# Kernel tuning notes

Measured on AMD Instinct MI355X. Metric: run time of the kernel, lower is better.

Reference implementation:

```python
import jax, jax.numpy as jnp
import numpy as np


def insert_tdl(tdl, x):
    # Shift delay line: newest sample at row 0, drop oldest row.
    return jnp.concatenate([x, tdl[:-1]], axis=0)


def setup_inputs() -> dict:
    key = jax.random.key(0)
    ks = jax.random.split(key, 17)
    B = 16384            # batch of parallel simulations (columns)
    H = 1024             # controller hidden size
    Hp = 1024            # plant hidden size
    Dci = Dcr = Dco = 64 # controller TDL depths
    Dpi = Dpo = 64       # plant TDL depths
    f = lambda k, s: jax.random.normal(k, s, dtype=jnp.float32)
    return {
        "reference": f(ks[0], (1, B)),
        "citdl": f(ks[1], (Dci, B)),
        "crtdl": f(ks[2], (Dcr, B)),
        "cotdl": f(ks[3], (Dco, B)),
        "pitdl": f(ks[4], (Dpi - 1, B)),  # fresh controller output a2 completes the line
        "potdl": f(ks[5], (Dpo, B)),
        # controller parameters (trainable in the original)
        "ciw": 0.01 * f(ks[6], (H, Dci)),
        "crw": 0.01 * f(ks[7], (H, Dcr)),
        "cow": 0.01 * f(ks[8], (H, Dco)),
        "cb1": 0.01 * f(ks[9], (H, 1)),
        "clw": 0.01 * f(ks[10], (1, H)),
        "cb2": 0.01 * f(ks[11], (1, 1)),
        # plant parameters (detached/frozen in the original)
        "piw": 0.01 * f(ks[12], (Hp, Dpi)),
        "p_ow": 0.01 * f(ks[13], (Hp, Dpo)),
        "pb1": 0.01 * f(ks[14], (Hp, 1)),
        "plw": 0.01 * f(ks[15], (1, Hp)),
        "pb2": 0.01 * f(ks[16], (1, 1)),
    }


def reference(reference, citdl, crtdl, cotdl, pitdl, potdl,
              ciw, crw, cow, cb1, clw, cb2,
              piw, p_ow, pb1, plw, pb2):
    # Controller MLP
    n1 = ciw @ citdl + crw @ crtdl + cow @ cotdl + cb1   # [H, B]
    a1 = jnp.tanh(n1)
    a2 = clw @ a1 + cb2                                   # [1, B] controller output
    # Plant MLP (frozen model of the plant)
    pdelay = jnp.concatenate([pitdl, a2], axis=0)         # [Dpi, B]
    n3 = piw @ pdelay + p_ow @ potdl + pb1                # [Hp, B]
    a3 = jnp.tanh(n3)
    a4 = plw @ a3 + pb2                                   # [1, B] plant output
    # TDL shift/insert updates
    citdl = insert_tdl(citdl, a2)
    crtdl = insert_tdl(crtdl, reference)
    cotdl = insert_tdl(cotdl, a4)
    pitdl = insert_tdl(pitdl, a2)
    potdl = insert_tdl(potdl, a4)
    return (a4, citdl, crtdl, cotdl, pitdl, potdl)
```

## Files before the change

kernel.cpp:

```cpp
#include <hip/hip_runtime.h>

#define B_COLS 16384
#define BT 64
#define NWAVES 8
#define NT 4
#define X1_STRIDE 200
#define X2_STRIDE 136

#define OFS_A4 0
#define OFS_CI 16384
#define OFS_CR 1064960
#define OFS_CO 2113536
#define OFS_PI 3162112
#define OFS_PO 4194304

#define W_CIW 0
#define W_CRW 65536
#define W_COW 131072
#define W_PIW 196608
#define W_POW 262144
#define W_TOTAL 327680

typedef short bf16x8_t __attribute__((ext_vector_type(8)));
typedef float f32x4_t __attribute__((ext_vector_type(4)));

__device__ __forceinline__ unsigned short bftrunc(float f) {
    return (unsigned short)(__float_as_uint(f) >> 16);
}
__device__ __forceinline__ unsigned int pk2(float lo, float hi) {
    return __builtin_amdgcn_perm(__float_as_uint(hi), __float_as_uint(lo), 0x07060302u);
}
__device__ __forceinline__ float tanh_fast(float x) {
    float x2 = x * x;
    float num = x * (15.0f + x2);
    float den = 15.0f + 6.0f * x2;
    return num * __builtin_amdgcn_rcpf(den);
}

extern "C" __global__ __launch_bounds__(256)
void prep_weights(const float* __restrict__ ciw, const float* __restrict__ crw,
                  const float* __restrict__ cow, const float* __restrict__ piw,
                  const float* __restrict__ p_ow, unsigned short* __restrict__ wbf)
{
    int idx8 = blockIdx.x * 256 + threadIdx.x;
    const float* src;
    int base = idx8 * 8;
    if      (idx8 < 8192)  { src = ciw  + base; }
    else if (idx8 < 16384) { src = crw  + base - W_CRW; }
    else if (idx8 < 24576) { src = cow  + base - W_COW; }
    else if (idx8 < 32768) { src = piw  + base - W_PIW; }
    else                   { src = p_ow + base - W_POW; }
    float4 a = *(const float4*)(src);
    float4 b = *(const float4*)(src + 4);
    uint4 o;
    o.x = pk2(a.x, a.y); o.y = pk2(a.z, a.w);
    o.z = pk2(b.x, b.y); o.w = pk2(b.z, b.w);
    *(uint4*)(wbf + base) = o;
}

template<bool BF16W>
__global__ __launch_bounds__(512, 2)
void fused_cell(const float* __restrict__ ref,
                const float* __restrict__ citdl,
                const float* __restrict__ crtdl,
                const float* __restrict__ cotdl,
                const float* __restrict__ pitdl,
                const float* __restrict__ potdl,
                const float* __restrict__ ciw,
                const float* __restrict__ crw,
                const float* __restrict__ cow,
                const float* __restrict__ cb1,
                const float* __restrict__ clw,
                const float* __restrict__ cb2,
                const float* __restrict__ piw,
                const float* __restrict__ p_ow,
                const float* __restrict__ pb1,
                const float* __restrict__ plw,
                const float* __restrict__ pb2,
                const unsigned short* __restrict__ wbf,
                float* __restrict__ out)
{
    __shared__ unsigned short X1T[BT * X1_STRIDE];
    __shared__ unsigned short X2T[BT * X2_STRIDE];
    __shared__ float redbuf1[NWAVES * BT];
    __shared__ float redbuf2[NWAVES * BT];
    __shared__ float pw63[1024];

    const int tid  = threadIdx.x;
    const int wave = tid >> 6;
    const int lane = tid & 63;
    const int quad = lane >> 4;
    const int l15  = lane & 15;
    const int c0   = blockIdx.x * BT;

    {
        const int rsub = tid >> 4;
        const int coff = (tid & 15) * 4;
        #pragma unroll
        for (int round = 0; round < 10; ++round) {
            const int g = round * 32 + rsub;
            const float* s; float* d; int k; int which;
            if (g < 192) {
                which = 0; k = g;
                if (g < 64)       {            s = citdl + (size_t)g * B_COLS;
                                    d = (g < 63) ? out + OFS_CI + (size_t)(g + 1) * B_COLS : nullptr; }
                else if (g < 128) { int r = g - 64;  s = crtdl + (size_t)r * B_COLS;
                                    d = (r < 63) ? out + OFS_CR + (size_t)(r + 1) * B_COLS : nullptr; }
                else              { int r = g - 128; s = cotdl + (size_t)r * B_COLS;
                                    d = (r < 63) ? out + OFS_CO + (size_t)(r + 1) * B_COLS : nullptr; }
            } else if (g < 255) {
                int r = g - 192; which = 1; k = r;
                s = pitdl + (size_t)r * B_COLS;
                d = (r < 62) ? out + OFS_PI + (size_t)(r + 1) * B_COLS : nullptr;
            } else if (g < 319) {
                int r = g - 255; which = 1; k = 64 + r;
                s = potdl + (size_t)r * B_COLS;
                d = (r < 63) ? out + OFS_PO + (size_t)(r + 1) * B_COLS : nullptr;
            } else {
                which = 2; k = 0; s = ref; d = out + OFS_CR;
            }
            float4 v = *(const float4*)(s + c0 + coff);
            if (d) *(float4*)(d + c0 + coff) = v;
            if (which == 0) {
                unsigned short* p = X1T + k;
                p[(coff + 0) * X1_STRIDE] = bftrunc(v.x);
                p[(coff + 1) * X1_STRIDE] = bftrunc(v.y);
                p[(coff + 2) * X1_STRIDE] = bftrunc(v.z);
                p[(coff + 3) * X1_STRIDE] = bftrunc(v.w);
            } else if (which == 1) {
                unsigned short* p = X2T + k;
                p[(coff + 0) * X2_STRIDE] = bftrunc(v.x);
                p[(coff + 1) * X2_STRIDE] = bftrunc(v.y);
                p[(coff + 2) * X2_STRIDE] = bftrunc(v.z);
                p[(coff + 3) * X2_STRIDE] = bftrunc(v.w);
            }
        }
        if (tid < BT) X2T[tid * X2_STRIDE + 63] = 0;
        for (int i = tid; i < 1024; i += 512) pw63[i] = piw[i * 64 + 63];
    }
    __syncthreads();

    float sc[NT] = {0.f, 0.f, 0.f, 0.f};
    {
        f32x4_t acc[8][NT];
        #pragma unroll
        for (int mt = 0; mt < 8; ++mt)
            #pragma unroll
            for (int nt = 0; nt < NT; ++nt) acc[mt][nt] = (f32x4_t){0.f, 0.f, 0.f, 0.f};

        #pragma unroll
        for (int kk = 0; kk < 6; ++kk) {
            bf16x8_t Bf[NT];
            #pragma unroll
            for (int nt = 0; nt < NT; ++nt)
                Bf[nt] = *(const bf16x8_t*)&X1T[(nt * 16 + l15) * X1_STRIDE + kk * 32 + quad * 8];
            #pragma unroll
            for (int mt = 0; mt < 8; ++mt) {
                const int rowA = wave * 128 + mt * 16 + l15;
                bf16x8_t a;
                if (BF16W) {
                    const unsigned short* wsrc = wbf + ((kk < 2) ? W_CIW : (kk < 4) ? W_CRW : W_COW);
                    a = *(const bf16x8_t*)(wsrc + (size_t)rowA * 64 + (kk & 1) * 32 + quad * 8);
                } else {
                    const float* wsrc = (kk < 2) ? ciw : (kk < 4) ? crw : cow;
                    const float* wp = wsrc + (size_t)rowA * 64 + (kk & 1) * 32 + quad * 8;
                    float4 a0 = *(const float4*)(wp);
                    float4 a1 = *(const float4*)(wp + 4);
                    union { bf16x8_t v; unsigned int u[4]; } A;
                    A.u[0] = pk2(a0.x, a0.y); A.u[1] = pk2(a0.z, a0.w);
                    A.u[2] = pk2(a1.x, a1.y); A.u[3] = pk2(a1.z, a1.w);
                    a = A.v;
                }
                #pragma unroll
                for (int nt = 0; nt < NT; ++nt)
                    acc[mt][nt] = __builtin_amdgcn_mfma_f32_16x16x32_bf16(a, Bf[nt], acc[mt][nt], 0, 0, 0);
            }
        }
        #pragma unroll
        for (int mt = 0; mt < 8; ++mt) {
            const int hr = wave * 128 + mt * 16 + quad * 4;
            float4 cb = *(const float4*)(cb1 + hr);
            float4 cl = *(const float4*)(clw + hr);
            const float cbv[4] = {cb.x, cb.y, cb.z, cb.w};
            const float clv[4] = {cl.x, cl.y, cl.z, cl.w};
            #pragma unroll
            for (int r = 0; r < 4; ++r)
                #pragma unroll
                for (int nt = 0; nt < NT; ++nt)
                    sc[nt] += clv[r] * tanh_fast(acc[mt][nt][r] + cbv[r]);
        }
    }
    #pragma unroll
    for (int nt = 0; nt < NT; ++nt) {
        sc[nt] += __shfl_xor(sc[nt], 16);
        sc[nt] += __shfl_xor(sc[nt], 32);
    }
    if (lane < 16)
        #pragma unroll
        for (int nt = 0; nt < NT; ++nt)
            redbuf1[wave * BT + nt * 16 + lane] = sc[nt];
    __syncthreads();

    const float cb2v = cb2[0];
    if (tid < BT) {
        float s = 0.f;
        #pragma unroll
        for (int w = 0; w < NWAVES; ++w) s += redbuf1[w * BT + tid];
        s += cb2v;
        out[OFS_CI + c0 + tid] = s;
        out[OFS_PI + c0 + tid] = s;
    }
    float a2v[NT];
    #pragma unroll
    for (int nt = 0; nt < NT; ++nt) {
        float s = 0.f;
        #pragma unroll
        for (int w = 0; w < NWAVES; ++w) s += redbuf1[w * BT + nt * 16 + l15];
        a2v[nt] = s + cb2v;
    }

    {
        f32x4_t acc[8][NT];
        #pragma unroll
        for (int mt = 0; mt < 8; ++mt)
            #pragma unroll
            for (int nt = 0; nt < NT; ++nt) acc[mt][nt] = (f32x4_t){0.f, 0.f, 0.f, 0.f};

        #pragma unroll
        for (int kk = 0; kk < 4; ++kk) {
            bf16x8_t Bf[NT];
            #pragma unroll
            for (int nt = 0; nt < NT; ++nt)
                Bf[nt] = *(const bf16x8_t*)&X2T[(nt * 16 + l15) * X2_STRIDE + kk * 32 + quad * 8];
            #pragma unroll
            for (int mt = 0; mt < 8; ++mt) {
                const int rowA = wave * 128 + mt * 16 + l15;
                bf16x8_t a;
                if (BF16W) {
                    const unsigned short* wsrc = wbf + ((kk < 2) ? W_PIW : W_POW);
                    a = *(const bf16x8_t*)(wsrc + (size_t)rowA * 64 + (kk & 1) * 32 + quad * 8);
                } else {
                    const float* wsrc = (kk < 2) ? piw : p_ow;
                    const float* wp = wsrc + (size_t)rowA * 64 + (kk & 1) * 32 + quad * 8;
                    float4 a0 = *(const float4*)(wp);
                    float4 a1 = *(const float4*)(wp + 4);
                    union { bf16x8_t v; unsigned int u[4]; } A;
                    A.u[0] = pk2(a0.x, a0.y); A.u[1] = pk2(a0.z, a0.w);
                    A.u[2] = pk2(a1.x, a1.y); A.u[3] = pk2(a1.z, a1.w);
                    a = A.v;
                }
                #pragma unroll
                for (int nt = 0; nt < NT; ++nt)
                    acc[mt][nt] = __builtin_amdgcn_mfma_f32_16x16x32_bf16(a, Bf[nt], acc[mt][nt], 0, 0, 0);
            }
        }
        float s4[NT] = {0.f, 0.f, 0.f, 0.f};
        #pragma unroll
        for (int mt = 0; mt < 8; ++mt) {
            const int hr = wave * 128 + mt * 16 + quad * 4;
            float4 pb = *(const float4*)(pb1 + hr);
            float4 pl = *(const float4*)(plw + hr);
            float4 pw = *(const float4*)(&pw63[hr]);
            const float pbv[4] = {pb.x, pb.y, pb.z, pb.w};
            const float plv[4] = {pl.x, pl.y, pl.z, pl.w};
            const float pwv[4] = {pw.x, pw.y, pw.z, pw.w};
            #pragma unroll
            for (int r = 0; r < 4; ++r)
                #pragma unroll
                for (int nt = 0; nt < NT; ++nt)
                    s4[nt] += plv[r] * tanh_fast(acc[mt][nt][r] + pbv[r] + pwv[r] * a2v[nt]);
        }
        #pragma unroll
        for (int nt = 0; nt < NT; ++nt) {
            s4[nt] += __shfl_xor(s4[nt], 16);
            s4[nt] += __shfl_xor(s4[nt], 32);
        }
        if (lane < 16)
            #pragma unroll
            for (int nt = 0; nt < NT; ++nt)
                redbuf2[wave * BT + nt * 16 + lane] = s4[nt];
    }
    __syncthreads();

    if (tid < BT) {
        float s = 0.f;
        #pragma unroll
        for (int w = 0; w < NWAVES; ++w) s += redbuf2[w * BT + tid];
        s += pb2[0];
        out[OFS_A4 + c0 + tid] = s;
        out[OFS_CO + c0 + tid] = s;
        out[OFS_PO + c0 + tid] = s;
    }
}

extern "C" void kernel_launch(void* const* d_in, const int* in_sizes, int n_in,
                              void* d_out, int out_size, void* d_ws, size_t ws_size,
                              hipStream_t stream) {
    (void)in_sizes; (void)n_in; (void)out_size;
    const float* ref   = (const float*)d_in[0];
    const float* citdl = (const float*)d_in[1];
    const float* crtdl = (const float*)d_in[2];
    const float* cotdl = (const float*)d_in[3];
    const float* pitdl = (const float*)d_in[4];
    const float* potdl = (const float*)d_in[5];
    const float* ciw   = (const float*)d_in[6];
    const float* crw   = (const float*)d_in[7];
    const float* cow   = (const float*)d_in[8];
    const float* cb1   = (const float*)d_in[9];
    const float* clw   = (const float*)d_in[10];
    const float* cb2   = (const float*)d_in[11];
    const float* piw   = (const float*)d_in[12];
    const float* p_ow  = (const float*)d_in[13];
    const float* pb1   = (const float*)d_in[14];
    const float* plw   = (const float*)d_in[15];
    const float* pb2   = (const float*)d_in[16];
    float* out = (float*)d_out;

    if (ws_size >= (size_t)W_TOTAL * 2) {
        unsigned short* wbf = (unsigned short*)d_ws;
        prep_weights<<<160, 256, 0, stream>>>(ciw, crw, cow, piw, p_ow, wbf);
        fused_cell<true><<<256, 512, 0, stream>>>(
            ref, citdl, crtdl, cotdl, pitdl, potdl,
            ciw, crw, cow, cb1, clw, cb2, piw, p_ow, pb1, plw, pb2,
            wbf, out);
    } else {
        fused_cell<false><<<256, 512, 0, stream>>>(
            ref, citdl, crtdl, cotdl, pitdl, potdl,
            ciw, crw, cow, cb1, clw, cb2, piw, p_ow, pb1, plw, pb2,
            nullptr, out);
    }
}
```

Before: 145.1 us.

## Restructure TDL staging to per-wave row-per-lane loads and batch LDS fragment reads

The staging phase now gives each lane one delay-line row and each wave an 8-column slice, replacing the 10-round generic loop with its branchy source selection. Each lane loads two float4s, copies them to the shifted output and writes the bf16 transpose into LDS. The MFMA loops now load B fragments for several k-steps at once so LDS reads are batched ahead of the MFMAs. Launch bounds drop from 2 to 1 blocks per SM, which frees registers but may lower occupancy. The new per-lane global accesses cover only 32 contiguous bytes per row, so coalescing is weaker than the old 16-lane 256-byte rows.

```diff
diff --git a/kernel.cpp b/kernel.cpp
--- a/kernel.cpp
+++ b/kernel.cpp
@@ -59,7 +59,7 @@
 }
 
 template<bool BF16W>
-__global__ __launch_bounds__(512, 2)
+__global__ __launch_bounds__(512, 1)
 void fused_cell(const float* __restrict__ ref,
                 const float* __restrict__ citdl,
                 const float* __restrict__ crtdl,
@@ -94,48 +94,69 @@
     const int c0   = blockIdx.x * BT;
 
     {
-        const int rsub = tid >> 4;
-        const int coff = (tid & 15) * 4;
-        #pragma unroll
-        for (int round = 0; round < 10; ++round) {
-            const int g = round * 32 + rsub;
-            const float* s; float* d; int k; int which;
-            if (g < 192) {
-                which = 0; k = g;
-                if (g < 64)       {            s = citdl + (size_t)g * B_COLS;
-                                    d = (g < 63) ? out + OFS_CI + (size_t)(g + 1) * B_COLS : nullptr; }
-                else if (g < 128) { int r = g - 64;  s = crtdl + (size_t)r * B_COLS;
-                                    d = (r < 63) ? out + OFS_CR + (size_t)(r + 1) * B_COLS : nullptr; }
-                else              { int r = g - 128; s = cotdl + (size_t)r * B_COLS;
-                                    d = (r < 63) ? out + OFS_CO + (size_t)(r + 1) * B_COLS : nullptr; }
-            } else if (g < 255) {
-                int r = g - 192; which = 1; k = r;
-                s = pitdl + (size_t)r * B_COLS;
-                d = (r < 62) ? out + OFS_PI + (size_t)(r + 1) * B_COLS : nullptr;
-            } else if (g < 319) {
-                int r = g - 255; which = 1; k = 64 + r;
-                s = potdl + (size_t)r * B_COLS;
-                d = (r < 63) ? out + OFS_PO + (size_t)(r + 1) * B_COLS : nullptr;
+        const int w8 = wave * 8;
+        #pragma unroll
+        for (int pass = 0; pass < 3; ++pass) {
+            const float* src = (pass == 0) ? citdl : (pass == 1) ? crtdl : cotdl;
+            float* dstb = out + ((pass == 0) ? OFS_CI : (pass == 1) ? OFS_CR : OFS_CO);
+            const int r = lane;
+            const int k = pass * 64 + lane;
+            const float* p = src + (size_t)r * B_COLS + c0 + w8;
+            float4 v0 = *(const float4*)(p);
+            float4 v1 = *(const float4*)(p + 4);
+            if (r < 63) {
+                float* q = dstb + (size_t)(r + 1) * B_COLS + c0 + w8;
+                *(float4*)(q) = v0;
+                *(float4*)(q + 4) = v1;
+            }
+            unsigned short* d16 = &X1T[w8 * X1_STRIDE + k];
+            d16[0 * X1_STRIDE] = bftrunc(v0.x); d16[1 * X1_STRIDE] = bftrunc(v0.y);
+            d16[2 * X1_STRIDE] = bftrunc(v0.z); d16[3 * X1_STRIDE] = bftrunc(v0.w);
+            d16[4 * X1_STRIDE] = bftrunc(v1.x); d16[5 * X1_STRIDE] = bftrunc(v1.y);
+            d16[6 * X1_STRIDE] = bftrunc(v1.z); d16[7 * X1_STRIDE] = bftrunc(v1.w);
+        }
+        {
+            const int r = lane;
+            if (r < 63) {
+                const float* p = pitdl + (size_t)r * B_COLS + c0 + w8;
+                float4 v0 = *(const float4*)(p);
+                float4 v1 = *(const float4*)(p + 4);
+                if (r < 62) {
+                    float* q = out + OFS_PI + (size_t)(r + 1) * B_COLS + c0 + w8;
+                    *(float4*)(q) = v0;
+                    *(float4*)(q + 4) = v1;
+                }
+                unsigned short* d16 = &X2T[w8 * X2_STRIDE + r];
+                d16[0 * X2_STRIDE] = bftrunc(v0.x); d16[1 * X2_STRIDE] = bftrunc(v0.y);
+                d16[2 * X2_STRIDE] = bftrunc(v0.z); d16[3 * X2_STRIDE] = bftrunc(v0.w);
+                d16[4 * X2_STRIDE] = bftrunc(v1.x); d16[5 * X2_STRIDE] = bftrunc(v1.y);
+                d16[6 * X2_STRIDE] = bftrunc(v1.z); d16[7 * X2_STRIDE] = bftrunc(v1.w);
             } else {
-                which = 2; k = 0; s = ref; d = out + OFS_CR;
-            }
-            float4 v = *(const float4*)(s + c0 + coff);
-            if (d) *(float4*)(d + c0 + coff) = v;
-            if (which == 0) {
-                unsigned short* p = X1T + k;
-                p[(coff + 0) * X1_STRIDE] = bftrunc(v.x);
-                p[(coff + 1) * X1_STRIDE] = bftrunc(v.y);
-                p[(coff + 2) * X1_STRIDE] = bftrunc(v.z);
-                p[(coff + 3) * X1_STRIDE] = bftrunc(v.w);
-            } else if (which == 1) {
-                unsigned short* p = X2T + k;
-                p[(coff + 0) * X2_STRIDE] = bftrunc(v.x);
-                p[(coff + 1) * X2_STRIDE] = bftrunc(v.y);
-                p[(coff + 2) * X2_STRIDE] = bftrunc(v.z);
-                p[(coff + 3) * X2_STRIDE] = bftrunc(v.w);
-            }
-        }
-        if (tid < BT) X2T[tid * X2_STRIDE + 63] = 0;
+                unsigned short* d16 = &X2T[w8 * X2_STRIDE + 63];
+                #pragma unroll
+                for (int i = 0; i < 8; ++i) d16[i * X2_STRIDE] = 0;
+            }
+        }
+        {
+            const int r = lane;
+            const float* p = potdl + (size_t)r * B_COLS + c0 + w8;
+            float4 v0 = *(const float4*)(p);
+            float4 v1 = *(const float4*)(p + 4);
+            if (r < 63) {
+                float* q = out + OFS_PO + (size_t)(r + 1) * B_COLS + c0 + w8;
+                *(float4*)(q) = v0;
+                *(float4*)(q + 4) = v1;
+            }
+            unsigned short* d16 = &X2T[w8 * X2_STRIDE + 64 + r];
+            d16[0 * X2_STRIDE] = bftrunc(v0.x); d16[1 * X2_STRIDE] = bftrunc(v0.y);
+            d16[2 * X2_STRIDE] = bftrunc(v0.z); d16[3 * X2_STRIDE] = bftrunc(v0.w);
+            d16[4 * X2_STRIDE] = bftrunc(v1.x); d16[5 * X2_STRIDE] = bftrunc(v1.y);
+            d16[6 * X2_STRIDE] = bftrunc(v1.z); d16[7 * X2_STRIDE] = bftrunc(v1.w);
+        }
+        if (tid < 16) {
+            float4 v = *(const float4*)(ref + c0 + tid * 4);
+            *(float4*)(out + OFS_CR + c0 + tid * 4) = v;
+        }
         for (int i = tid; i < 1024; i += 512) pw63[i] = piw[i * 64 + 63];
     }
     __syncthreads();
@@ -149,31 +170,38 @@
             for (int nt = 0; nt < NT; ++nt) acc[mt][nt] = (f32x4_t){0.f, 0.f, 0.f, 0.f};
 
         #pragma unroll
-        for (int kk = 0; kk < 6; ++kk) {
-            bf16x8_t Bf[NT];
-            #pragma unroll
-            for (int nt = 0; nt < NT; ++nt)
-                Bf[nt] = *(const bf16x8_t*)&X1T[(nt * 16 + l15) * X1_STRIDE + kk * 32 + quad * 8];
-            #pragma unroll
-            for (int mt = 0; mt < 8; ++mt) {
-                const int rowA = wave * 128 + mt * 16 + l15;
-                bf16x8_t a;
-                if (BF16W) {
-                    const unsigned short* wsrc = wbf + ((kk < 2) ? W_CIW : (kk < 4) ? W_CRW : W_COW);
-                    a = *(const bf16x8_t*)(wsrc + (size_t)rowA * 64 + (kk & 1) * 32 + quad * 8);
-                } else {
-                    const float* wsrc = (kk < 2) ? ciw : (kk < 4) ? crw : cow;
-                    const float* wp = wsrc + (size_t)rowA * 64 + (kk & 1) * 32 + quad * 8;
-                    float4 a0 = *(const float4*)(wp);
-                    float4 a1 = *(const float4*)(wp + 4);
-                    union { bf16x8_t v; unsigned int u[4]; } A;
-                    A.u[0] = pk2(a0.x, a0.y); A.u[1] = pk2(a0.z, a0.w);
-                    A.u[2] = pk2(a1.x, a1.y); A.u[3] = pk2(a1.z, a1.w);
-                    a = A.v;
+        for (int half = 0; half < 2; ++half) {
+            bf16x8_t Bf[3][NT];
+            #pragma unroll
+            for (int kk = 0; kk < 3; ++kk)
+                #pragma unroll
+                for (int nt = 0; nt < NT; ++nt)
+                    Bf[kk][nt] = *(const bf16x8_t*)&X1T[(nt * 16 + l15) * X1_STRIDE
+                                                        + (half * 3 + kk) * 32 + quad * 8];
+            #pragma unroll
+            for (int kk = 0; kk < 3; ++kk) {
+                const int kg = half * 3 + kk;
+                #pragma unroll
+                for (int mt = 0; mt < 8; ++mt) {
+                    const int rowA = wave * 128 + mt * 16 + l15;
+                    bf16x8_t a;
+                    if (BF16W) {
+                        const unsigned short* wsrc = wbf + ((kg < 2) ? W_CIW : (kg < 4) ? W_CRW : W_COW);
+                        a = *(const bf16x8_t*)(wsrc + (size_t)rowA * 64 + (kg & 1) * 32 + quad * 8);
+                    } else {
+                        const float* wsrc = (kg < 2) ? ciw : (kg < 4) ? crw : cow;
+                        const float* wp = wsrc + (size_t)rowA * 64 + (kg & 1) * 32 + quad * 8;
+                        float4 a0 = *(const float4*)(wp);
+                        float4 a1 = *(const float4*)(wp + 4);
+                        union { bf16x8_t v; unsigned int u[4]; } A;
+                        A.u[0] = pk2(a0.x, a0.y); A.u[1] = pk2(a0.z, a0.w);
+                        A.u[2] = pk2(a1.x, a1.y); A.u[3] = pk2(a1.z, a1.w);
+                        a = A.v;
+                    }
+                    #pragma unroll
+                    for (int nt = 0; nt < NT; ++nt)
+                        acc[mt][nt] = __builtin_amdgcn_mfma_f32_16x16x32_bf16(a, Bf[kk][nt], acc[mt][nt], 0, 0, 0);
                 }
-                #pragma unroll
-                for (int nt = 0; nt < NT; ++nt)
-                    acc[mt][nt] = __builtin_amdgcn_mfma_f32_16x16x32_bf16(a, Bf[nt], acc[mt][nt], 0, 0, 0);
             }
         }
         #pragma unroll
@@ -227,31 +255,38 @@
             for (int nt = 0; nt < NT; ++nt) acc[mt][nt] = (f32x4_t){0.f, 0.f, 0.f, 0.f};
 
         #pragma unroll
-        for (int kk = 0; kk < 4; ++kk) {
-            bf16x8_t Bf[NT];
-            #pragma unroll
-            for (int nt = 0; nt < NT; ++nt)
-                Bf[nt] = *(const bf16x8_t*)&X2T[(nt * 16 + l15) * X2_STRIDE + kk * 32 + quad * 8];
-            #pragma unroll
-            for (int mt = 0; mt < 8; ++mt) {
-                const int rowA = wave * 128 + mt * 16 + l15;
-                bf16x8_t a;
-                if (BF16W) {
-                    const unsigned short* wsrc = wbf + ((kk < 2) ? W_PIW : W_POW);
-                    a = *(const bf16x8_t*)(wsrc + (size_t)rowA * 64 + (kk & 1) * 32 + quad * 8);
-                } else {
-                    const float* wsrc = (kk < 2) ? piw : p_ow;
-                    const float* wp = wsrc + (size_t)rowA * 64 + (kk & 1) * 32 + quad * 8;
-                    float4 a0 = *(const float4*)(wp);
-                    float4 a1 = *(const float4*)(wp + 4);
-                    union { bf16x8_t v; unsigned int u[4]; } A;
-                    A.u[0] = pk2(a0.x, a0.y); A.u[1] = pk2(a0.z, a0.w);
-                    A.u[2] = pk2(a1.x, a1.y); A.u[3] = pk2(a1.z, a1.w);
-                    a = A.v;
+        for (int half = 0; half < 2; ++half) {
+            bf16x8_t Bf[2][NT];
+            #pragma unroll
+            for (int kk = 0; kk < 2; ++kk)
+                #pragma unroll
+                for (int nt = 0; nt < NT; ++nt)
+                    Bf[kk][nt] = *(const bf16x8_t*)&X2T[(nt * 16 + l15) * X2_STRIDE
+                                                        + (half * 2 + kk) * 32 + quad * 8];
+            #pragma unroll
+            for (int kk = 0; kk < 2; ++kk) {
+                const int kg = half * 2 + kk;
+                #pragma unroll
+                for (int mt = 0; mt < 8; ++mt) {
+                    const int rowA = wave * 128 + mt * 16 + l15;
+                    bf16x8_t a;
+                    if (BF16W) {
+                        const unsigned short* wsrc = wbf + ((kg < 2) ? W_PIW : W_POW);
+                        a = *(const bf16x8_t*)(wsrc + (size_t)rowA * 64 + (kg & 1) * 32 + quad * 8);
+                    } else {
+                        const float* wsrc = (kg < 2) ? piw : p_ow;
+                        const float* wp = wsrc + (size_t)rowA * 64 + (kg & 1) * 32 + quad * 8;
+                        float4 a0 = *(const float4*)(wp);
+                        float4 a1 = *(const float4*)(wp + 4);
+                        union { bf16x8_t v; unsigned int u[4]; } A;
+                        A.u[0] = pk2(a0.x, a0.y); A.u[1] = pk2(a0.z, a0.w);
+                        A.u[2] = pk2(a1.x, a1.y); A.u[3] = pk2(a1.z, a1.w);
+                        a = A.v;
+                    }
+                    #pragma unroll
+                    for (int nt = 0; nt < NT; ++nt)
+                        acc[mt][nt] = __builtin_amdgcn_mfma_f32_16x16x32_bf16(a, Bf[kk][nt], acc[mt][nt], 0, 0, 0);
                 }
-                #pragma unroll
-                for (int nt = 0; nt < NT; ++nt)
-                    acc[mt][nt] = __builtin_amdgcn_mfma_f32_16x16x32_bf16(a, Bf[nt], acc[mt][nt], 0, 0, 0);
             }
         }
         float s4[NT] = {0.f, 0.f, 0.f, 0.f};
```

New measurement: 144.1 us. No clear change (-0.6%).

## Use 1024-thread blocks, halve per-wave M tiles, hoist plant GEMM before barrier

Applied to the files above, without the earlier changes.

Doubles the block to 16 waves, each covering 64 hidden rows instead of 128, which halves accumulator register use and raises the number of waves in flight. The staging loop is rewritten so that each wave loads a 4-column strip for every TDL row in one pass, replacing the branchy per-round row assignment. The plant GEMM, which does not depend on a2, now runs before the barrier that waits on the controller reduction, so it can overlap with that synchronisation. The cost is a larger reduction over more waves and 1024-thread blocks, and the new staging pattern issues narrower 16-byte-per-lane loads across rows.

```diff
diff --git a/kernel.cpp b/kernel.cpp
--- a/kernel.cpp
+++ b/kernel.cpp
@@ -2,8 +2,9 @@
 
 #define B_COLS 16384
 #define BT 64
-#define NWAVES 8
+#define NWAVES 16
 #define NT 4
+#define MT 4
 #define X1_STRIDE 200
 #define X2_STRIDE 136
 
@@ -59,7 +60,7 @@
 }
 
 template<bool BF16W>
-__global__ __launch_bounds__(512, 2)
+__global__ __launch_bounds__(1024, 4)
 void fused_cell(const float* __restrict__ ref,
                 const float* __restrict__ citdl,
                 const float* __restrict__ crtdl,
@@ -94,57 +95,59 @@
     const int c0   = blockIdx.x * BT;
 
     {
-        const int rsub = tid >> 4;
-        const int coff = (tid & 15) * 4;
-        #pragma unroll
-        for (int round = 0; round < 10; ++round) {
-            const int g = round * 32 + rsub;
-            const float* s; float* d; int k; int which;
-            if (g < 192) {
-                which = 0; k = g;
-                if (g < 64)       {            s = citdl + (size_t)g * B_COLS;
-                                    d = (g < 63) ? out + OFS_CI + (size_t)(g + 1) * B_COLS : nullptr; }
-                else if (g < 128) { int r = g - 64;  s = crtdl + (size_t)r * B_COLS;
-                                    d = (r < 63) ? out + OFS_CR + (size_t)(r + 1) * B_COLS : nullptr; }
-                else              { int r = g - 128; s = cotdl + (size_t)r * B_COLS;
-                                    d = (r < 63) ? out + OFS_CO + (size_t)(r + 1) * B_COLS : nullptr; }
-            } else if (g < 255) {
-                int r = g - 192; which = 1; k = r;
-                s = pitdl + (size_t)r * B_COLS;
-                d = (r < 62) ? out + OFS_PI + (size_t)(r + 1) * B_COLS : nullptr;
-            } else if (g < 319) {
-                int r = g - 255; which = 1; k = 64 + r;
-                s = potdl + (size_t)r * B_COLS;
-                d = (r < 63) ? out + OFS_PO + (size_t)(r + 1) * B_COLS : nullptr;
-            } else {
-                which = 2; k = 0; s = ref; d = out + OFS_CR;
-            }
-            float4 v = *(const float4*)(s + c0 + coff);
-            if (d) *(float4*)(d + c0 + coff) = v;
-            if (which == 0) {
-                unsigned short* p = X1T + k;
-                p[(coff + 0) * X1_STRIDE] = bftrunc(v.x);
-                p[(coff + 1) * X1_STRIDE] = bftrunc(v.y);
-                p[(coff + 2) * X1_STRIDE] = bftrunc(v.z);
-                p[(coff + 3) * X1_STRIDE] = bftrunc(v.w);
-            } else if (which == 1) {
-                unsigned short* p = X2T + k;
-                p[(coff + 0) * X2_STRIDE] = bftrunc(v.x);
-                p[(coff + 1) * X2_STRIDE] = bftrunc(v.y);
-                p[(coff + 2) * X2_STRIDE] = bftrunc(v.z);
-                p[(coff + 3) * X2_STRIDE] = bftrunc(v.w);
-            }
-        }
-        if (tid < BT) X2T[tid * X2_STRIDE + 63] = 0;
-        for (int i = tid; i < 1024; i += 512) pw63[i] = piw[i * 64 + 63];
+        const int w4 = wave * 4;
+        const int r  = lane;
+        #pragma unroll
+        for (int pass = 0; pass < 3; ++pass) {
+            const float* src = (pass == 0) ? citdl : (pass == 1) ? crtdl : cotdl;
+            float* dstb = out + ((pass == 0) ? OFS_CI : (pass == 1) ? OFS_CR : OFS_CO);
+            const int k = pass * 64 + r;
+            float4 v = *(const float4*)(src + (size_t)r * B_COLS + c0 + w4);
+            if (r < 63)
+                *(float4*)(dstb + (size_t)(r + 1) * B_COLS + c0 + w4) = v;
+            unsigned short* d16 = &X1T[w4 * X1_STRIDE + k];
+            d16[0 * X1_STRIDE] = bftrunc(v.x);
+            d16[1 * X1_STRIDE] = bftrunc(v.y);
+            d16[2 * X1_STRIDE] = bftrunc(v.z);
+            d16[3 * X1_STRIDE] = bftrunc(v.w);
+        }
+        if (r < 63) {
+            float4 v = *(const float4*)(pitdl + (size_t)r * B_COLS + c0 + w4);
+            if (r < 62)
+                *(float4*)(out + OFS_PI + (size_t)(r + 1) * B_COLS + c0 + w4) = v;
+            unsigned short* d16 = &X2T[w4 * X2_STRIDE + r];
+            d16[0 * X2_STRIDE] = bftrunc(v.x);
+            d16[1 * X2_STRIDE] = bftrunc(v.y);
+            d16[2 * X2_STRIDE] = bftrunc(v.z);
+            d16[3 * X2_STRIDE] = bftrunc(v.w);
+        } else {
+            unsigned short* d16 = &X2T[w4 * X2_STRIDE + 63];
+            #pragma unroll
+            for (int i = 0; i < 4; ++i) d16[i * X2_STRIDE] = 0;
+        }
+        {
+            float4 v = *(const float4*)(potdl + (size_t)r * B_COLS + c0 + w4);
+            if (r < 63)
+                *(float4*)(out + OFS_PO + (size_t)(r + 1) * B_COLS + c0 + w4) = v;
+            unsigned short* d16 = &X2T[w4 * X2_STRIDE + 64 + r];
+            d16[0 * X2_STRIDE] = bftrunc(v.x);
+            d16[1 * X2_STRIDE] = bftrunc(v.y);
+            d16[2 * X2_STRIDE] = bftrunc(v.z);
+            d16[3 * X2_STRIDE] = bftrunc(v.w);
+        }
+        if (tid < 16) {
+            float4 v = *(const float4*)(ref + c0 + tid * 4);
+            *(float4*)(out + OFS_CR + c0 + tid * 4) = v;
+        }
+        pw63[tid] = piw[tid * 64 + 63];
     }
     __syncthreads();
 
     float sc[NT] = {0.f, 0.f, 0.f, 0.f};
     {
-        f32x4_t acc[8][NT];
-        #pragma unroll
-        for (int mt = 0; mt < 8; ++mt)
+        f32x4_t acc[MT][NT];
+        #pragma unroll
+        for (int mt = 0; mt < MT; ++mt)
             #pragma unroll
             for (int nt = 0; nt < NT; ++nt) acc[mt][nt] = (f32x4_t){0.f, 0.f, 0.f, 0.f};
 
@@ -155,8 +158,8 @@
             for (int nt = 0; nt < NT; ++nt)
                 Bf[nt] = *(const bf16x8_t*)&X1T[(nt * 16 + l15) * X1_STRIDE + kk * 32 + quad * 8];
             #pragma unroll
-            for (int mt = 0; mt < 8; ++mt) {
-                const int rowA = wave * 128 + mt * 16 + l15;
+            for (int mt = 0; mt < MT; ++mt) {
+                const int rowA = wave * 64 + mt * 16 + l15;
                 bf16x8_t a;
                 if (BF16W) {
                     const unsigned short* wsrc = wbf + ((kk < 2) ? W_CIW : (kk < 4) ? W_CRW : W_COW);
@@ -177,8 +180,8 @@
             }
         }
         #pragma unroll
-        for (int mt = 0; mt < 8; ++mt) {
-            const int hr = wave * 128 + mt * 16 + quad * 4;
+        for (int mt = 0; mt < MT; ++mt) {
+            const int hr = wave * 64 + mt * 16 + quad * 4;
             float4 cb = *(const float4*)(cb1 + hr);
             float4 cl = *(const float4*)(clw + hr);
             const float cbv[4] = {cb.x, cb.y, cb.z, cb.w};
@@ -199,6 +202,41 @@
         #pragma unroll
         for (int nt = 0; nt < NT; ++nt)
             redbuf1[wave * BT + nt * 16 + lane] = sc[nt];
+
+    f32x4_t acc2[MT][NT];
+    #pragma unroll
+    for (int mt = 0; mt < MT; ++mt)
+        #pragma unroll
+        for (int nt = 0; nt < NT; ++nt) acc2[mt][nt] = (f32x4_t){0.f, 0.f, 0.f, 0.f};
+
+    #pragma unroll
+    for (int kk = 0; kk < 4; ++kk) {
+        bf16x8_t Bf[NT];
+        #pragma unroll
+        for (int nt = 0; nt < NT; ++nt)
+            Bf[nt] = *(const bf16x8_t*)&X2T[(nt * 16 + l15) * X2_STRIDE + kk * 32 + quad * 8];
+        #pragma unroll
+        for (int mt = 0; mt < MT; ++mt) {
+            const int rowA = wave * 64 + mt * 16 + l15;
+            bf16x8_t a;
+            if (BF16W) {
+                const unsigned short* wsrc = wbf + ((kk < 2) ? W_PIW : W_POW);
+                a = *(const bf16x8_t*)(wsrc + (size_t)rowA * 64 + (kk & 1) * 32 + quad * 8);
+            } else {
+                const float* wsrc = (kk < 2) ? piw : p_ow;
+                const float* wp = wsrc + (size_t)rowA * 64 + (kk & 1) * 32 + quad * 8;
+                float4 a0 = *(const float4*)(wp);
+                float4 a1 = *(const float4*)(wp + 4);
+                union { bf16x8_t v; unsigned int u[4]; } A;
+                A.u[0] = pk2(a0.x, a0.y); A.u[1] = pk2(a0.z, a0.w);
+                A.u[2] = pk2(a1.x, a1.y); A.u[3] = pk2(a1.z, a1.w);
+                a = A.v;
+            }
+            #pragma unroll
+            for (int nt = 0; nt < NT; ++nt)
+                acc2[mt][nt] = __builtin_amdgcn_mfma_f32_16x16x32_bf16(a, Bf[nt], acc2[mt][nt], 0, 0, 0);
+        }
+    }
     __syncthreads();
 
     const float cb2v = cb2[0];
@@ -220,44 +258,10 @@
     }
 
     {
-        f32x4_t acc[8][NT];
-        #pragma unroll
-        for (int mt = 0; mt < 8; ++mt)
-            #pragma unroll
-            for (int nt = 0; nt < NT; ++nt) acc[mt][nt] = (f32x4_t){0.f, 0.f, 0.f, 0.f};
-
-        #pragma unroll
-        for (int kk = 0; kk < 4; ++kk) {
-            bf16x8_t Bf[NT];
-            #pragma unroll
-            for (int nt = 0; nt < NT; ++nt)
-                Bf[nt] = *(const bf16x8_t*)&X2T[(nt * 16 + l15) * X2_STRIDE + kk * 32 + quad * 8];
-            #pragma unroll
-            for (int mt = 0; mt < 8; ++mt) {
-                const int rowA = wave * 128 + mt * 16 + l15;
-                bf16x8_t a;
-                if (BF16W) {
-                    const unsigned short* wsrc = wbf + ((kk < 2) ? W_PIW : W_POW);
-                    a = *(const bf16x8_t*)(wsrc + (size_t)rowA * 64 + (kk & 1) * 32 + quad * 8);
-                } else {
-                    const float* wsrc = (kk < 2) ? piw : p_ow;
-                    const float* wp = wsrc + (size_t)rowA * 64 + (kk & 1) * 32 + quad * 8;
-                    float4 a0 = *(const float4*)(wp);
-                    float4 a1 = *(const float4*)(wp + 4);
-                    union { bf16x8_t v; unsigned int u[4]; } A;
-                    A.u[0] = pk2(a0.x, a0.y); A.u[1] = pk2(a0.z, a0.w);
-                    A.u[2] = pk2(a1.x, a1.y); A.u[3] = pk2(a1.z, a1.w);
-                    a = A.v;
-                }
-                #pragma unroll
-                for (int nt = 0; nt < NT; ++nt)
-                    acc[mt][nt] = __builtin_amdgcn_mfma_f32_16x16x32_bf16(a, Bf[nt], acc[mt][nt], 0, 0, 0);
-            }
-        }
         float s4[NT] = {0.f, 0.f, 0.f, 0.f};
         #pragma unroll
-        for (int mt = 0; mt < 8; ++mt) {
-            const int hr = wave * 128 + mt * 16 + quad * 4;
+        for (int mt = 0; mt < MT; ++mt) {
+            const int hr = wave * 64 + mt * 16 + quad * 4;
             float4 pb = *(const float4*)(pb1 + hr);
             float4 pl = *(const float4*)(plw + hr);
             float4 pw = *(const float4*)(&pw63[hr]);
@@ -268,7 +272,7 @@
             for (int r = 0; r < 4; ++r)
                 #pragma unroll
                 for (int nt = 0; nt < NT; ++nt)
-                    s4[nt] += plv[r] * tanh_fast(acc[mt][nt][r] + pbv[r] + pwv[r] * a2v[nt]);
+                    s4[nt] += plv[r] * tanh_fast(acc2[mt][nt][r] + pbv[r] + pwv[r] * a2v[nt]);
         }
         #pragma unroll
         for (int nt = 0; nt < NT; ++nt) {
@@ -319,12 +323,12 @@
     if (ws_size >= (size_t)W_TOTAL * 2) {
         unsigned short* wbf = (unsigned short*)d_ws;
         prep_weights<<<160, 256, 0, stream>>>(ciw, crw, cow, piw, p_ow, wbf);
-        fused_cell<true><<<256, 512, 0, stream>>>(
+        fused_cell<true><<<256, 1024, 0, stream>>>(
             ref, citdl, crtdl, cotdl, pitdl, potdl,
             ciw, crw, cow, cb1, clw, cb2, piw, p_ow, pb1, plw, pb2,
             wbf, out);
     } else {
-        fused_cell<false><<<256, 512, 0, stream>>>(
+        fused_cell<false><<<256, 1024, 0, stream>>>(
             ref, citdl, crtdl, cotdl, pitdl, potdl,
             ciw, crw, cow, cb1, clw, cb2, piw, p_ow, pb1, plw, pb2,
             nullptr, out);
```

Result: faster. 140.6 us (-3.1%).
